# Optimization experiments

Measured on AMD Instinct MI355X. Metric: run time of the kernel, lower is better.

## Reference

```python
import jax, jax.numpy as jnp
import numpy as np

B, S, D_MODEL, H = 2, 2048, 512, 8
D_HEAD = D_MODEL // H  # 64; d_qk == d_model here


def setup_inputs() -> dict:
    key = jax.random.key(0)
    ks = jax.random.split(key, 7)
    sc = 1.0 / np.sqrt(D_MODEL)
    return {
        "x": jax.random.normal(ks[0], (B, S, D_MODEL), dtype=jnp.float32),
        "Wqk_w": jax.random.normal(ks[1], (2 * D_MODEL, D_MODEL), dtype=jnp.float32) * sc,
        "Wqk_b": jax.random.normal(ks[2], (2 * D_MODEL,), dtype=jnp.float32) * 0.01,
        "Wv_w": jax.random.normal(ks[3], (D_MODEL, D_MODEL), dtype=jnp.float32) * sc,
        "Wv_b": jax.random.normal(ks[4], (D_MODEL,), dtype=jnp.float32) * 0.01,
        "Wo_w": jax.random.normal(ks[5], (D_MODEL, D_MODEL), dtype=jnp.float32) * sc,
        "Wo_b": jax.random.normal(ks[6], (D_MODEL,), dtype=jnp.float32) * 0.01,
    }


def reference(x, Wqk_w, Wqk_b, Wv_w, Wv_b, Wo_w, Wo_b):
    b, s, _ = x.shape
    # projections
    qk = x @ Wqk_w.T + Wqk_b              # [B,S,2*d_qk]
    v = x @ Wv_w.T + Wv_b                 # [B,S,d_model]
    qk = qk.reshape(b, s, 2, H, D_HEAD)   # (two h d) layout
    v = v.reshape(b, s, H, D_HEAD)
    q, k = qk[:, :, 0], qk[:, :, 1]
    # generalized linear attention feature map: elu(x)+1
    q = jax.nn.elu(q) + 1.0
    k = jax.nn.elu(k) + 1.0
    scores = jnp.einsum('bthd,bshd->bhts', q, k)          # [B,H,T,S]
    mask = jnp.tril(jnp.ones((s, s), dtype=scores.dtype))  # causal multiplicative mask
    scores = scores * mask
    nu = scores.sum(axis=-1, keepdims=True)               # row normalizer
    attention = scores / nu
    context = jnp.einsum('bhts,bshd->bthd', attention, v)  # [B,T,H,D]
    out = context.reshape(b, s, D_MODEL) @ Wo_w.T + Wo_b
    return out
```

## Files before the change

### kernel.cpp

```cpp
#include <hip/hip_runtime.h>
#include <math.h>

#define B_N 2
#define S_N 2048
#define DM  512
#define H_N 8
#define DH  64
#define NC  32
#define CH  64

typedef __bf16 bf16x8 __attribute__((ext_vector_type(8)));
typedef float  f32x4  __attribute__((ext_vector_type(4)));

__device__ __forceinline__ unsigned short f2bf(float f) {
    unsigned int u = __float_as_uint(f);
    u += 0x7FFFu + ((u >> 16) & 1u);
    return (unsigned short)(u >> 16);
}

__device__ __forceinline__ void gload16(const void* g, void* l) {
    __builtin_amdgcn_global_load_lds(
        (const __attribute__((address_space(1))) unsigned int*)g,
        (__attribute__((address_space(3))) unsigned int*)l, 16, 0, 0);
}

__global__ __launch_bounds__(256) void convert_bf16(
    const float* __restrict__ x,  const float* __restrict__ wqk,
    const float* __restrict__ wv, const float* __restrict__ wo,
    unsigned short* __restrict__ xb,  unsigned short* __restrict__ wqkb,
    unsigned short* __restrict__ wvb, unsigned short* __restrict__ wob)
{
    int gid = blockIdx.x * 256 + threadIdx.x;
    const float* src; unsigned short* dst; int off;
    if (gid < 524288)      { src = x;   dst = xb;   off = gid; }
    else if (gid < 655360) { src = wqk; dst = wqkb; off = gid - 524288; }
    else if (gid < 720896) { src = wv;  dst = wvb;  off = gid - 655360; }
    else                   { src = wo;  dst = wob;  off = gid - 720896; }
    float4 v = ((const float4*)src)[off];
    ushort4 r; r.x = f2bf(v.x); r.y = f2bf(v.y); r.z = f2bf(v.z); r.w = f2bf(v.w);
    ((ushort4*)dst)[off] = r;
}

__global__ __launch_bounds__(256) void gemm_qkv_fused(
    const unsigned short* __restrict__ xb,
    const unsigned short* __restrict__ Wqkb,
    const unsigned short* __restrict__ Wvb,
    const float* __restrict__ bqk, const float* __restrict__ bv,
    unsigned short* __restrict__ qb, unsigned short* __restrict__ kb_,
    unsigned short* __restrict__ vtb,
    float* __restrict__ Asum, float* __restrict__ zsum)
{
    __shared__ unsigned short Alds[64 * 32];
    __shared__ unsigned short Blds[128 * 32];
    __shared__ unsigned short ktT[64 * 72];
    __shared__ unsigned short vtT[64 * 72];

    const int tid = threadIdx.x;
    const int w = tid >> 6, l = tid & 63;
    const int wm = w >> 1, wn = w & 1;
    const int lane15 = l & 15, quad = l >> 4;
    const int bx = blockIdx.x;
    const int m0 = blockIdx.y * 64;
    const int isq = (bx < 4);
    const int h = isq ? 0 : (bx - 4);

    const int srow = w * 16 + (l >> 2);
    const int skof = (l & 3) << 3;

    f32x4 acc[2][4];
    #pragma unroll
    for (int i = 0; i < 2; i++)
        #pragma unroll
        for (int j = 0; j < 4; j++) acc[i][j] = (f32x4){0.f, 0.f, 0.f, 0.f};

    for (int k0 = 0; k0 < DM; k0 += 32) {
        __syncthreads();
        gload16(&xb[(size_t)(m0 + srow) * DM + k0 + skof], (char*)Alds + w * 1024);
        if (isq) {
            gload16(&Wqkb[(size_t)(bx * 128 + srow) * DM + k0 + skof],      (char*)Blds + w * 1024);
            gload16(&Wqkb[(size_t)(bx * 128 + 64 + srow) * DM + k0 + skof], (char*)Blds + 4096 + w * 1024);
        } else {
            gload16(&Wqkb[(size_t)(512 + h * 64 + srow) * DM + k0 + skof],  (char*)Blds + w * 1024);
            gload16(&Wvb[(size_t)(h * 64 + srow) * DM + k0 + skof],         (char*)Blds + 4096 + w * 1024);
        }
        __syncthreads();

        bf16x8 af[2], bfr[4];
        #pragma unroll
        for (int i = 0; i < 2; i++)
            af[i] = *(bf16x8*)&Alds[(wm * 32 + i * 16 + lane15) * 32 + quad * 8];
        #pragma unroll
        for (int j = 0; j < 4; j++)
            bfr[j] = *(bf16x8*)&Blds[(wn * 64 + j * 16 + lane15) * 32 + quad * 8];
        #pragma unroll
        for (int i = 0; i < 2; i++)
            #pragma unroll
            for (int j = 0; j < 4; j++)
                acc[i][j] = __builtin_amdgcn_mfma_f32_16x16x32_bf16(af[i], bfr[j], acc[i][j], 0, 0, 0);
    }

    const int bbu = m0 >> 11;
    const int t0  = m0 & (S_N - 1);
    const int c0  = t0 >> 6;

    if (isq) {
        #pragma unroll
        for (int i = 0; i < 2; i++) {
            #pragma unroll
            for (int rg = 0; rg < 4; rg++) {
                int m = m0 + wm * 32 + i * 16 + quad * 4 + rg;
                int bb = m >> 11, t = m & (S_N - 1);
                #pragma unroll
                for (int j = 0; j < 4; j++) {
                    int n = bx * 128 + wn * 64 + j * 16 + lane15;
                    float val = acc[i][j][rg] + bqk[n];
                    val = (val > 0.f) ? (val + 1.f) : __expf(val);
                    qb[(((size_t)bb * H_N + (n >> 6)) * S_N + t) * DH + (n & 63)] = f2bf(val);
                }
            }
        }
        return;
    }

    #pragma unroll
    for (int i = 0; i < 2; i++) {
        #pragma unroll
        for (int rg = 0; rg < 4; rg++) {
            int tl = wm * 32 + i * 16 + quad * 4 + rg;
            int t  = t0 + tl;
            #pragma unroll
            for (int j = 0; j < 4; j++) {
                int col = j * 16 + lane15;
                if (wn == 0) {
                    float val = acc[i][j][rg] + bqk[512 + h * 64 + col];
                    val = (val > 0.f) ? (val + 1.f) : __expf(val);
                    unsigned short us = f2bf(val);
                    kb_[(((size_t)bbu * H_N + h) * S_N + t) * DH + col] = us;
                    ktT[col * 72 + tl] = us;
                } else {
                    float val = acc[i][j][rg] + bv[h * 64 + col];
                    vtT[col * 72 + tl] = f2bf(val);
                }
            }
        }
    }
    __syncthreads();

    {
        size_t vbase = (((size_t)bbu * H_N + h) * DH) * S_N + t0;
        #pragma unroll
        for (int it = 0; it < 2; it++) {
            int idx = it * 2048 + tid * 8;
            int d = idx >> 6, tt = idx & 63;
            *(bf16x8*)&vtb[vbase + (size_t)d * S_N + tt] = *(bf16x8*)&vtT[d * 72 + tt];
        }
    }

    {
        int blk = ((bbu * H_N + h) * NC) + c0;
        bf16x8 va[2];
        #pragma unroll
        for (int s = 0; s < 2; s++)
            va[s] = *(bf16x8*)&vtT[(w * 16 + lane15) * 72 + s * 32 + quad * 8];
        f32x4 sacc[4];
        #pragma unroll
        for (int j = 0; j < 4; j++) sacc[j] = (f32x4){0.f, 0.f, 0.f, 0.f};
        #pragma unroll
        for (int j = 0; j < 4; j++)
            #pragma unroll
            for (int s = 0; s < 2; s++) {
                bf16x8 kB = *(bf16x8*)&ktT[(j * 16 + lane15) * 72 + s * 32 + quad * 8];
                sacc[j] = __builtin_amdgcn_mfma_f32_16x16x32_bf16(va[s], kB, sacc[j], 0, 0, 0);
            }
        #pragma unroll
        for (int j = 0; j < 4; j++)
            #pragma unroll
            for (int rg = 0; rg < 4; rg++)
                Asum[(size_t)blk * 4096 + (w * 16 + quad * 4 + rg) * 64 + j * 16 + lane15] = sacc[j][rg];
    }

    if (tid < 64) {
        float z = 0.f;
        #pragma unroll
        for (int p = 0; p < 8; p++) {
            bf16x8 kk = *(bf16x8*)&ktT[tid * 72 + p * 8];
            #pragma unroll
            for (int e = 0; e < 8; e++) z += (float)kk[e];
        }
        zsum[(size_t)((bbu * H_N + h) * NC + c0) * 64 + tid] = z;
    }
}

__global__ __launch_bounds__(256) void scan_states(
    const float* __restrict__ Asum, float* __restrict__ zsum,
    unsigned short* __restrict__ Sptb)
{
    const int gid = blockIdx.x * 256 + threadIdx.x;
    const int bh = gid / 4160;
    const int r  = gid % 4160;
    if (r < 4096) {
        size_t base = (size_t)bh * NC * 4096 + r;
        float vals[NC];
        #pragma unroll
        for (int c = 0; c < NC; c++) vals[c] = Asum[base + (size_t)c * 4096];
        float acc = 0.f;
        #pragma unroll
        for (int c = 0; c < NC; c++) {
            float tmp = vals[c];
            Sptb[base + (size_t)c * 4096] = f2bf(acc);
            acc += tmp;
        }
    } else {
        int d = r - 4096;
        size_t base = (size_t)bh * NC * 64 + d;
        float vals[NC];
        #pragma unroll
        for (int c = 0; c < NC; c++) vals[c] = zsum[base + (size_t)c * 64];
        float acc = 0.f;
        #pragma unroll
        for (int c = 0; c < NC; c++) {
            float tmp = vals[c];
            zsum[base + (size_t)c * 64] = acc;
            acc += tmp;
        }
    }
}

__global__ __launch_bounds__(256) void attn_mfma(
    const unsigned short* __restrict__ qb, const unsigned short* __restrict__ kb_,
    const unsigned short* __restrict__ vtb, const unsigned short* __restrict__ Sptb,
    const float* __restrict__ zsum, unsigned short* __restrict__ ctxb)
{
    __shared__ __align__(16) unsigned short P[64 * 72];
    __shared__ float nupart[64][4];

    const int blk = blockIdx.x;
    const int bh = blk >> 5, c = blk & 31;
    const int b = bh >> 3, h = bh & 7;
    const int tid = threadIdx.x;
    const int w = tid >> 6, l = tid & 63;
    const int lane15 = l & 15, quad = l >> 4;

    const unsigned short* qc  = qb  + (size_t)bh * S_N * DH + c * CH * DH;
    const unsigned short* kc  = kb_ + (size_t)bh * S_N * DH + c * CH * DH;
    const unsigned short* vtc = vtb + (size_t)bh * DH * S_N + c * CH;
    const unsigned short* spc = Sptb + (size_t)blk * 4096;
    const float* zc = zsum + (size_t)blk * 64;

    bf16x8 af[2];
    #pragma unroll
    for (int s = 0; s < 2; s++)
        af[s] = *(const bf16x8*)&qc[(w * 16 + lane15) * DH + s * 32 + quad * 8];

    f32x4 sacc[4];
    #pragma unroll
    for (int j = 0; j < 4; j++) sacc[j] = (f32x4){0.f, 0.f, 0.f, 0.f};
    #pragma unroll
    for (int j = 0; j < 4; j++)
        #pragma unroll
        for (int s = 0; s < 2; s++) {
            bf16x8 bk = *(const bf16x8*)&kc[(j * 16 + lane15) * DH + s * 32 + quad * 8];
            sacc[j] = __builtin_amdgcn_mfma_f32_16x16x32_bf16(af[s], bk, sacc[j], 0, 0, 0);
        }

    const int r0 = w * 16 + quad * 4;
    #pragma unroll
    for (int j = 0; j < 4; j++) {
        int u = j * 16 + lane15;
        #pragma unroll
        for (int rg = 0; rg < 4; rg++) {
            int rr = r0 + rg;
            float v = (u <= rr) ? sacc[j][rg] : 0.f;
            P[rr * 72 + u] = f2bf(v);
        }
    }
    __syncthreads();

    const int tl = tid >> 2, part = tid & 3;
    float nup = 0.f;
    {
        bf16x8 p0 = *(const bf16x8*)&P[tl * 72 + part * 16];
        bf16x8 p1 = *(const bf16x8*)&P[tl * 72 + part * 16 + 8];
        bf16x8 q0 = *(const bf16x8*)&qc[tl * DH + part * 16];
        bf16x8 q1 = *(const bf16x8*)&qc[tl * DH + part * 16 + 8];
        #pragma unroll
        for (int i = 0; i < 8; i++) {
            nup += (float)p0[i] + (float)p1[i];
            nup += (float)q0[i] * zc[part * 16 + i];
            nup += (float)q1[i] * zc[part * 16 + 8 + i];
        }
    }
    nupart[tl][part] = nup;
    __syncthreads();

    bf16x8 pa[2];
    #pragma unroll
    for (int s = 0; s < 2; s++)
        pa[s] = *(const bf16x8*)&P[(w * 16 + lane15) * 72 + s * 32 + quad * 8];

    f32x4 acc[4];
    #pragma unroll
    for (int j = 0; j < 4; j++) acc[j] = (f32x4){0.f, 0.f, 0.f, 0.f};
    #pragma unroll
    for (int j = 0; j < 4; j++)
        #pragma unroll
        for (int s = 0; s < 2; s++) {
            bf16x8 bv = *(const bf16x8*)&vtc[(size_t)(j * 16 + lane15) * S_N + s * 32 + quad * 8];
            acc[j] = __builtin_amdgcn_mfma_f32_16x16x32_bf16(pa[s], bv, acc[j], 0, 0, 0);
            bf16x8 bs = *(const bf16x8*)&spc[(j * 16 + lane15) * 64 + s * 32 + quad * 8];
            acc[j] = __builtin_amdgcn_mfma_f32_16x16x32_bf16(af[s], bs, acc[j], 0, 0, 0);
        }

    #pragma unroll
    for (int rg = 0; rg < 4; rg++) {
        int rr = r0 + rg;
        float nu = nupart[rr][0] + nupart[rr][1] + nupart[rr][2] + nupart[rr][3];
        float inv = 1.f / nu;
        size_t obase = ((size_t)b * S_N + c * CH + rr) * DM + h * DH;
        #pragma unroll
        for (int j = 0; j < 4; j++)
            ctxb[obase + j * 16 + lane15] = f2bf(acc[j][rg] * inv);
    }
}

__global__ __launch_bounds__(256) void gemm_out_mfma(
    const unsigned short* __restrict__ ctxb,
    const unsigned short* __restrict__ Wob,
    const float* __restrict__ bo, float* __restrict__ out)
{
    __shared__ unsigned short Alds[64 * 32];
    __shared__ unsigned short Blds[64 * 32];
    const int tid = threadIdx.x;
    const int w = tid >> 6, l = tid & 63;
    const int wm = w >> 1, wn = w & 1;
    const int lane15 = l & 15, quad = l >> 4;
    const int n0 = blockIdx.x * 64;
    const int m0 = blockIdx.y * 64;

    const int srow = w * 16 + (l >> 2);
    const int skof = (l & 3) << 3;

    f32x4 acc[2][2];
    #pragma unroll
    for (int i = 0; i < 2; i++)
        #pragma unroll
        for (int j = 0; j < 2; j++) acc[i][j] = (f32x4){0.f, 0.f, 0.f, 0.f};

    for (int k0 = 0; k0 < DM; k0 += 32) {
        __syncthreads();
        gload16(&ctxb[(size_t)(m0 + srow) * DM + k0 + skof], (char*)Alds + w * 1024);
        gload16(&Wob[(size_t)(n0 + srow) * DM + k0 + skof],  (char*)Blds + w * 1024);
        __syncthreads();

        bf16x8 af[2], bfr[2];
        #pragma unroll
        for (int i = 0; i < 2; i++)
            af[i] = *(bf16x8*)&Alds[(wm * 32 + i * 16 + lane15) * 32 + quad * 8];
        #pragma unroll
        for (int j = 0; j < 2; j++)
            bfr[j] = *(bf16x8*)&Blds[(wn * 32 + j * 16 + lane15) * 32 + quad * 8];
        #pragma unroll
        for (int i = 0; i < 2; i++)
            #pragma unroll
            for (int j = 0; j < 2; j++)
                acc[i][j] = __builtin_amdgcn_mfma_f32_16x16x32_bf16(af[i], bfr[j], acc[i][j], 0, 0, 0);
    }

    #pragma unroll
    for (int i = 0; i < 2; i++) {
        #pragma unroll
        for (int rg = 0; rg < 4; rg++) {
            int m = m0 + wm * 32 + i * 16 + quad * 4 + rg;
            #pragma unroll
            for (int j = 0; j < 2; j++) {
                int n = n0 + wn * 32 + j * 16 + lane15;
                out[(size_t)m * DM + n] = acc[i][j][rg] + bo[n];
            }
        }
    }
}

extern "C" void kernel_launch(void* const* d_in, const int* in_sizes, int n_in,
                              void* d_out, int out_size, void* d_ws, size_t ws_size,
                              hipStream_t stream)
{
    const float* x   = (const float*)d_in[0];
    const float* Wqk = (const float*)d_in[1];
    const float* bqk = (const float*)d_in[2];
    const float* Wv  = (const float*)d_in[3];
    const float* bv  = (const float*)d_in[4];
    const float* Wo  = (const float*)d_in[5];
    const float* bo  = (const float*)d_in[6];
    float* out = (float*)d_out;

    const size_t NTOK = (size_t)B_N * S_N * DM;
    float* Asum = (float*)d_ws;
    float* zsum = Asum + NTOK;
    unsigned short* xb   = (unsigned short*)(zsum + 32768);
    unsigned short* Wqkb = xb   + NTOK;
    unsigned short* Wvb  = Wqkb + 524288;
    unsigned short* Wob  = Wvb  + 262144;
    unsigned short* qb   = Wob  + 262144;
    unsigned short* kb_  = qb   + NTOK;
    unsigned short* vtb  = kb_  + NTOK;
    unsigned short* Sptb = vtb  + NTOK;
    unsigned short* ctxb = Sptb + NTOK;

    convert_bf16  <<<dim3(3072),   256, 0, stream>>>(x, Wqk, Wv, Wo, xb, Wqkb, Wvb, Wob);
    gemm_qkv_fused<<<dim3(12, 64), 256, 0, stream>>>(xb, Wqkb, Wvb, bqk, bv, qb, kb_, vtb, Asum, zsum);
    scan_states   <<<dim3(260),    256, 0, stream>>>(Asum, zsum, Sptb);
    attn_mfma     <<<dim3(512),    256, 0, stream>>>(qb, kb_, vtb, Sptb, zsum, ctxb);
    gemm_out_mfma <<<dim3(8, 64),  256, 0, stream>>>(ctxb, Wob, bo, out);
}
```

Baseline: 115.2 us.

## Load GEMM operands directly from global memory instead of staging through LDS

In both the fused QKV projection GEMM and the output projection GEMM, the LDS staging buffers and the two per-iteration barriers are removed. Each wave now loads its MFMA fragments straight from global memory into registers, and the k-loop is unrolled by 4. This removes barrier stalls and LDS round-trips so that more loads can be in flight. In exchange, operands shared between waves are loaded redundantly, now four per-lane 16-byte strided row reads per tile where staging used one coalesced load, and caching is left to L1/L2.

```diff
diff --git a/kernel.cpp b/kernel.cpp
--- a/kernel.cpp
+++ b/kernel.cpp
@@ -16,12 +16,6 @@
     unsigned int u = __float_as_uint(f);
     u += 0x7FFFu + ((u >> 16) & 1u);
     return (unsigned short)(u >> 16);
-}
-
-__device__ __forceinline__ void gload16(const void* g, void* l) {
-    __builtin_amdgcn_global_load_lds(
-        (const __attribute__((address_space(1))) unsigned int*)g,
-        (__attribute__((address_space(3))) unsigned int*)l, 16, 0, 0);
 }
 
 __global__ __launch_bounds__(256) void convert_bf16(
@@ -50,8 +44,6 @@
     unsigned short* __restrict__ vtb,
     float* __restrict__ Asum, float* __restrict__ zsum)
 {
-    __shared__ unsigned short Alds[64 * 32];
-    __shared__ unsigned short Blds[128 * 32];
     __shared__ unsigned short ktT[64 * 72];
     __shared__ unsigned short vtT[64 * 72];
 
@@ -64,8 +56,16 @@
     const int isq = (bx < 4);
     const int h = isq ? 0 : (bx - 4);
 
-    const int srow = w * 16 + (l >> 2);
-    const int skof = (l & 3) << 3;
+    const unsigned short* arow0 = xb + (size_t)(m0 + wm * 32 + lane15) * DM;
+    const unsigned short* arow1 = arow0 + 16 * DM;
+    const unsigned short* brow[4];
+    #pragma unroll
+    for (int j = 0; j < 4; j++) {
+        int r = wn * 64 + j * 16 + lane15;
+        if (isq)        brow[j] = Wqkb + (size_t)(bx * 128 + r) * DM;
+        else if (wn == 0) brow[j] = Wqkb + (size_t)(512 + h * 64 + j * 16 + lane15) * DM;
+        else              brow[j] = Wvb  + (size_t)(h * 64 + j * 16 + lane15) * DM;
+    }
 
     f32x4 acc[2][4];
     #pragma unroll
@@ -73,30 +73,23 @@
         #pragma unroll
         for (int j = 0; j < 4; j++) acc[i][j] = (f32x4){0.f, 0.f, 0.f, 0.f};
 
+    const int ko = quad * 8;
+    #pragma unroll 4
     for (int k0 = 0; k0 < DM; k0 += 32) {
-        __syncthreads();
-        gload16(&xb[(size_t)(m0 + srow) * DM + k0 + skof], (char*)Alds + w * 1024);
-        if (isq) {
-            gload16(&Wqkb[(size_t)(bx * 128 + srow) * DM + k0 + skof],      (char*)Blds + w * 1024);
-            gload16(&Wqkb[(size_t)(bx * 128 + 64 + srow) * DM + k0 + skof], (char*)Blds + 4096 + w * 1024);
-        } else {
-            gload16(&Wqkb[(size_t)(512 + h * 64 + srow) * DM + k0 + skof],  (char*)Blds + w * 1024);
-            gload16(&Wvb[(size_t)(h * 64 + srow) * DM + k0 + skof],         (char*)Blds + 4096 + w * 1024);
-        }
-        __syncthreads();
-
-        bf16x8 af[2], bfr[4];
-        #pragma unroll
-        for (int i = 0; i < 2; i++)
-            af[i] = *(bf16x8*)&Alds[(wm * 32 + i * 16 + lane15) * 32 + quad * 8];
-        #pragma unroll
-        for (int j = 0; j < 4; j++)
-            bfr[j] = *(bf16x8*)&Blds[(wn * 64 + j * 16 + lane15) * 32 + quad * 8];
-        #pragma unroll
-        for (int i = 0; i < 2; i++)
-            #pragma unroll
-            for (int j = 0; j < 4; j++)
-                acc[i][j] = __builtin_amdgcn_mfma_f32_16x16x32_bf16(af[i], bfr[j], acc[i][j], 0, 0, 0);
+        bf16x8 a0 = *(const bf16x8*)&arow0[k0 + ko];
+        bf16x8 a1 = *(const bf16x8*)&arow1[k0 + ko];
+        bf16x8 b0 = *(const bf16x8*)&brow[0][k0 + ko];
+        bf16x8 b1 = *(const bf16x8*)&brow[1][k0 + ko];
+        bf16x8 b2 = *(const bf16x8*)&brow[2][k0 + ko];
+        bf16x8 b3 = *(const bf16x8*)&brow[3][k0 + ko];
+        acc[0][0] = __builtin_amdgcn_mfma_f32_16x16x32_bf16(a0, b0, acc[0][0], 0, 0, 0);
+        acc[0][1] = __builtin_amdgcn_mfma_f32_16x16x32_bf16(a0, b1, acc[0][1], 0, 0, 0);
+        acc[0][2] = __builtin_amdgcn_mfma_f32_16x16x32_bf16(a0, b2, acc[0][2], 0, 0, 0);
+        acc[0][3] = __builtin_amdgcn_mfma_f32_16x16x32_bf16(a0, b3, acc[0][3], 0, 0, 0);
+        acc[1][0] = __builtin_amdgcn_mfma_f32_16x16x32_bf16(a1, b0, acc[1][0], 0, 0, 0);
+        acc[1][1] = __builtin_amdgcn_mfma_f32_16x16x32_bf16(a1, b1, acc[1][1], 0, 0, 0);
+        acc[1][2] = __builtin_amdgcn_mfma_f32_16x16x32_bf16(a1, b2, acc[1][2], 0, 0, 0);
+        acc[1][3] = __builtin_amdgcn_mfma_f32_16x16x32_bf16(a1, b3, acc[1][3], 0, 0, 0);
     }
 
     const int bbu = m0 >> 11;
@@ -305,8 +298,8 @@
     for (int j = 0; j < 4; j++)
         #pragma unroll
         for (int s = 0; s < 2; s++) {
-            bf16x8 bv = *(const bf16x8*)&vtc[(size_t)(j * 16 + lane15) * S_N + s * 32 + quad * 8];
-            acc[j] = __builtin_amdgcn_mfma_f32_16x16x32_bf16(pa[s], bv, acc[j], 0, 0, 0);
+            bf16x8 bv8 = *(const bf16x8*)&vtc[(size_t)(j * 16 + lane15) * S_N + s * 32 + quad * 8];
+            acc[j] = __builtin_amdgcn_mfma_f32_16x16x32_bf16(pa[s], bv8, acc[j], 0, 0, 0);
             bf16x8 bs = *(const bf16x8*)&spc[(j * 16 + lane15) * 64 + s * 32 + quad * 8];
             acc[j] = __builtin_amdgcn_mfma_f32_16x16x32_bf16(af[s], bs, acc[j], 0, 0, 0);
         }
@@ -328,8 +321,6 @@
     const unsigned short* __restrict__ Wob,
     const float* __restrict__ bo, float* __restrict__ out)
 {
-    __shared__ unsigned short Alds[64 * 32];
-    __shared__ unsigned short Blds[64 * 32];
     const int tid = threadIdx.x;
     const int w = tid >> 6, l = tid & 63;
     const int wm = w >> 1, wn = w & 1;
@@ -337,8 +328,10 @@
     const int n0 = blockIdx.x * 64;
     const int m0 = blockIdx.y * 64;
 
-    const int srow = w * 16 + (l >> 2);
-    const int skof = (l & 3) << 3;
+    const unsigned short* arow0 = ctxb + (size_t)(m0 + wm * 32 + lane15) * DM;
+    const unsigned short* arow1 = arow0 + 16 * DM;
+    const unsigned short* brow0 = Wob + (size_t)(n0 + wn * 32 + lane15) * DM;
+    const unsigned short* brow1 = brow0 + 16 * DM;
 
     f32x4 acc[2][2];
     #pragma unroll
@@ -346,24 +339,17 @@
         #pragma unroll
         for (int j = 0; j < 2; j++) acc[i][j] = (f32x4){0.f, 0.f, 0.f, 0.f};
 
+    const int ko = quad * 8;
+    #pragma unroll 4
     for (int k0 = 0; k0 < DM; k0 += 32) {
-        __syncthreads();
-        gload16(&ctxb[(size_t)(m0 + srow) * DM + k0 + skof], (char*)Alds + w * 1024);
-        gload16(&Wob[(size_t)(n0 + srow) * DM + k0 + skof],  (char*)Blds + w * 1024);
-        __syncthreads();
-
-        bf16x8 af[2], bfr[2];
-        #pragma unroll
-        for (int i = 0; i < 2; i++)
-            af[i] = *(bf16x8*)&Alds[(wm * 32 + i * 16 + lane15) * 32 + quad * 8];
-        #pragma unroll
-        for (int j = 0; j < 2; j++)
-            bfr[j] = *(bf16x8*)&Blds[(wn * 32 + j * 16 + lane15) * 32 + quad * 8];
-        #pragma unroll
-        for (int i = 0; i < 2; i++)
-            #pragma unroll
-            for (int j = 0; j < 2; j++)
-                acc[i][j] = __builtin_amdgcn_mfma_f32_16x16x32_bf16(af[i], bfr[j], acc[i][j], 0, 0, 0);
+        bf16x8 a0 = *(const bf16x8*)&arow0[k0 + ko];
+        bf16x8 a1 = *(const bf16x8*)&arow1[k0 + ko];
+        bf16x8 b0 = *(const bf16x8*)&brow0[k0 + ko];
+        bf16x8 b1 = *(const bf16x8*)&brow1[k0 + ko];
+        acc[0][0] = __builtin_amdgcn_mfma_f32_16x16x32_bf16(a0, b0, acc[0][0], 0, 0, 0);
+        acc[0][1] = __builtin_amdgcn_mfma_f32_16x16x32_bf16(a0, b1, acc[0][1], 0, 0, 0);
+        acc[1][0] = __builtin_amdgcn_mfma_f32_16x16x32_bf16(a1, b0, acc[1][0], 0, 0, 0);
+        acc[1][1] = __builtin_amdgcn_mfma_f32_16x16x32_bf16(a1, b1, acc[1][1], 0, 0, 0);
     }
 
     #pragma unroll
```

After: 145.6 us. 26.4% more time.
